# Kernel optimization log

Measured on AMD Instinct MI355X. Metric: run time of the kernel, lower is better.

Reference implementation:

```python
import jax, jax.numpy as jnp
import numpy as np

B, NPG, DEG = 16, 2048, 16          # graphs, nodes per graph, avg degree
N_TOT = B * NPG
E_TOT = N_TOT * DEG
NEG_SLOPE = 0.2


def _gat(x, src, dst, n, w, a_src, a_dst, b):
    # PyG GATConv: concat heads, add self loops, leaky_relu(0.2), segment softmax over targets
    H, C = a_src.shape
    h = (x @ w.T).reshape(n, H, C)                       # [n,H,C]
    sl = jnp.arange(n, dtype=src.dtype)
    s = jnp.concatenate([src, sl])
    d = jnp.concatenate([dst, sl])
    e = jax.nn.leaky_relu((h * a_src).sum(-1)[s] + (h * a_dst).sum(-1)[d], NEG_SLOPE)  # [E+n,H]
    emax = jax.lax.stop_gradient(jax.ops.segment_max(e, d, num_segments=n))
    ee = jnp.exp(e - emax[d])
    alpha = ee / (jax.ops.segment_sum(ee, d, num_segments=n)[d] + 1e-16)
    out = jax.ops.segment_sum(alpha[:, :, None] * h[s], d, num_segments=n)  # [n,H,C]
    return out.reshape(n, H * C) + b


def _gcn(x, src, dst, mask, n, w, b):
    # PyG GCNConv with self loops + symmetric norm; mask = float edge validity
    h = x @ w.T
    deg = jax.ops.segment_sum(mask, dst, num_segments=n) + 1.0  # +1 for self loop
    dinv = jax.lax.rsqrt(deg)
    coef = dinv[src] * dinv[dst] * mask
    out = jax.ops.segment_sum(coef[:, None] * h[src], dst, num_segments=n) + (dinv * dinv)[:, None] * h
    return out + b


def _sag(x, src, dst, mask, b_graphs, npg, k, w_rel, b_rel, w_root):
    # PyG SAGPooling(ratio=0.5): GraphConv score, per-graph top-k, x[perm]*tanh(score[perm]), filter_adj
    n = b_graphs * npg
    agg = jax.ops.segment_sum(mask[:, None] * x[src], dst, num_segments=n)
    score = (agg @ w_rel.T + b_rel + x @ w_root.T)[:, 0]      # [n]
    _, idx = jax.lax.top_k(score.reshape(b_graphs, npg), k)    # [B,k]
    perm = (jnp.arange(b_graphs, dtype=jnp.int32)[:, None] * npg + idx).reshape(-1)
    x_new = x[perm] * jnp.tanh(score[perm])[:, None]
    new_id = jnp.full((n,), -1, jnp.int32).at[perm].set(jnp.arange(b_graphs * k, dtype=jnp.int32))
    ns, nd = new_id[src], new_id[dst]
    valid = mask * ((ns >= 0) & (nd >= 0)).astype(x.dtype)
    return x_new, jnp.maximum(ns, 0), jnp.maximum(nd, 0), valid


def setup_inputs() -> dict:
    key = jax.random.key(0)
    ks = jax.random.split(key, 32)

    def lin(k, o, i):
        return (jax.random.normal(k, (o, i), jnp.float32) / np.sqrt(i)).astype(jnp.float32)

    x = jax.random.normal(ks[0], (N_TOT, 64), jnp.float32)
    off = jnp.repeat(jnp.arange(B, dtype=jnp.int32) * NPG, NPG * DEG)
    src = off + jax.random.randint(ks[1], (E_TOT,), 0, NPG, jnp.int32)
    dst = off + jax.random.randint(ks[2], (E_TOT,), 0, NPG, jnp.int32)
    edge_index = jnp.stack([src, dst])
    batch = jnp.repeat(jnp.arange(B, dtype=jnp.int32), NPG)

    return {
        'x': x, 'edge_index': edge_index, 'batch': batch,
        'gat1_w': lin(ks[3], 256, 64), 'gat1_asrc': lin(ks[4], 4, 64), 'gat1_adst': lin(ks[5], 4, 64),
        'gat1_b': jnp.zeros((256,), jnp.float32),
        'gat2_w': lin(ks[6], 256, 256), 'gat2_asrc': lin(ks[7], 4, 64), 'gat2_adst': lin(ks[8], 4, 64),
        'gat2_b': jnp.zeros((256,), jnp.float32),
        # pooling GCN1: 256 -> 128
        'gcn1_w': lin(ks[9], 128, 256), 'gcn1_b': jnp.zeros((128,), jnp.float32),
        'sag1_wrel': lin(ks[10], 1, 128), 'sag1_brel': jnp.zeros((1,), jnp.float32), 'sag1_wroot': lin(ks[11], 1, 128),
        # pooling GCN2: 128 -> 128
        'gcn2_w': lin(ks[12], 128, 128), 'gcn2_b': jnp.zeros((128,), jnp.float32),
        'sag2_wrel': lin(ks[13], 1, 128), 'sag2_brel': jnp.zeros((1,), jnp.float32), 'sag2_wroot': lin(ks[14], 1, 128),
        # classifier 128 -> 256 -> 128 -> 10
        'fc1_w': lin(ks[15], 256, 128), 'fc1_b': jnp.zeros((256,), jnp.float32),
        'fc2_w': lin(ks[16], 128, 256), 'fc2_b': jnp.zeros((128,), jnp.float32),
        'out_w': lin(ks[17], 10, 128), 'out_b': jnp.zeros((10,), jnp.float32),
    }


def reference(x, edge_index, batch,
              gat1_w, gat1_asrc, gat1_adst, gat1_b,
              gat2_w, gat2_asrc, gat2_adst, gat2_b,
              gcn1_w, gcn1_b, sag1_wrel, sag1_brel, sag1_wroot,
              gcn2_w, gcn2_b, sag2_wrel, sag2_brel, sag2_wroot,
              fc1_w, fc1_b, fc2_w, fc2_b, out_w, out_b):
    n = x.shape[0]
    src, dst = edge_index[0], edge_index[1]
    ones = jnp.ones(src.shape[0], x.dtype)

    # GAT encoder
    h = jax.nn.relu(_gat(x, src, dst, n, gat1_w, gat1_asrc, gat1_adst, gat1_b))
    h = _gat(h, src, dst, n, gat2_w, gat2_asrc, gat2_adst, gat2_b)  # [n,256]

    # GCN + SAGPool x2
    h = jax.nn.relu(_gcn(h, src, dst, ones, n, gcn1_w, gcn1_b))
    k1 = NPG // 2
    h, s1, d1, m1 = _sag(h, src, dst, ones, B, NPG, k1, sag1_wrel, sag1_brel, sag1_wroot)
    h = jax.nn.relu(_gcn(h, s1, d1, m1, B * k1, gcn2_w, gcn2_b))
    k2 = k1 // 2
    h, s2, d2, m2 = _sag(h, s1, d1, m1, B, k1, k2, sag2_wrel, sag2_brel, sag2_wroot)

    # global mean pool (equal-size graphs -> simple reshape-mean; batch vec implied)
    g = h.reshape(B, k2, -1).mean(axis=1)  # [B,128]

    # classifier MLP
    g = jax.nn.relu(g @ fc1_w.T + fc1_b)
    g = jax.nn.relu(g @ fc2_w.T + fc2_b)
    return g @ out_w.T + out_b  # [B,10]
```

## Files before the change

### kernel.cpp

```cpp
#include <hip/hip_runtime.h>

#define N1 32768
#define EE 524288
#define NB 16
#define DEG 16
#define NPG1 2048
#define KK1 1024
#define N2 16384
#define NPG2 1024
#define KK2 512
#define N3 8192

typedef _Float16 half8_t __attribute__((ext_vector_type(8)));
typedef float floatx16 __attribute__((ext_vector_type(16)));

static __device__ __forceinline__ float leaky(float x){ return fmaxf(x, 0.2f*x); }

__global__ void count_dst(const int* __restrict__ dst, int* __restrict__ cnt, int E){
    int i = blockIdx.x*blockDim.x + threadIdx.x;
    if (i < E) atomicAdd(&cnt[dst[i]], 1);
}

__global__ void remap_count(const int* __restrict__ src, const int* __restrict__ dst,
                            const int* __restrict__ nid, int* __restrict__ ns,
                            int* __restrict__ nd, int* __restrict__ cnt, int E){
    int i = blockIdx.x*blockDim.x + threadIdx.x;
    if (i < E){
        int a = nid[src[i]], b = nid[dst[i]];
        ns[i] = a; nd[i] = b;
        if (a >= 0 && b >= 0) atomicAdd(&cnt[b], 1);
    }
}

__global__ void blocksum_k(const int* __restrict__ cnt, int* __restrict__ bs){
    __shared__ int red[4];
    int tid = threadIdx.x;
    int v = cnt[blockIdx.x*256 + tid];
    #pragma unroll
    for (int off = 32; off; off >>= 1) v += __shfl_xor(v, off);
    if ((tid & 63) == 0) red[tid >> 6] = v;
    __syncthreads();
    if (tid == 0) bs[blockIdx.x] = red[0] + red[1] + red[2] + red[3];
}

__global__ void scan_write_k(const int* __restrict__ cnt, const int* __restrict__ bs,
                             int nb, int2* __restrict__ rpx, int* __restrict__ cur,
                             float* __restrict__ dinv){
    __shared__ int sbs[128];
    __shared__ int wsum[4];
    int tid = threadIdx.x;
    int b = blockIdx.x;
    if (tid < nb) sbs[tid] = bs[tid];
    __syncthreads();
    for (int off = 1; off < nb; off <<= 1){
        int v = 0;
        if (tid < nb && tid >= off) v = sbs[tid - off];
        __syncthreads();
        if (tid < nb) sbs[tid] += v;
        __syncthreads();
    }
    int base = (b == 0) ? 0 : sbs[b-1];
    int i = b*256 + tid;
    int c = cnt[i];
    int lane = tid & 63, wv = tid >> 6;
    int x = c;
    #pragma unroll
    for (int off = 1; off < 64; off <<= 1){ int y = __shfl_up(x, off); if (lane >= off) x += y; }
    if (lane == 63) wsum[wv] = x;
    __syncthreads();
    if (tid == 0){ int run = 0; for (int w2 = 0; w2 < 4; w2++){ int t = wsum[w2]; wsum[w2] = run; run += t; } }
    __syncthreads();
    int excl = x - c + wsum[wv];
    int beg = base + excl;
    rpx[i]  = make_int2(beg, beg + c);
    cur[i]  = beg;
    dinv[i] = rsqrtf((float)c + 1.0f);
}

__global__ void scatter1(const int* __restrict__ src, const int* __restrict__ dst,
                         int* __restrict__ cur, int* __restrict__ esrc, int E){
    int i = blockIdx.x*blockDim.x + threadIdx.x;
    if (i < E){ int p = atomicAdd(&cur[dst[i]], 1); esrc[p] = src[i]; }
}

__global__ void scatter2(const int* __restrict__ ns, const int* __restrict__ nd,
                         int* __restrict__ cur, int* __restrict__ esrc, int E){
    int i = blockIdx.x*blockDim.x + threadIdx.x;
    if (i < E){
        int a = ns[i], b = nd[i];
        if (a >= 0 && b >= 0){ int p = atomicAdd(&cur[b], 1); esrc[p] = a; }
    }
}

__global__ void wsplit4(const float* __restrict__ w0, int n0,
                        const float* __restrict__ w1, int n1,
                        const float* __restrict__ w2, int n2,
                        const float* __restrict__ w3, int n3,
                        _Float16* __restrict__ wh, _Float16* __restrict__ wl){
    int i = blockIdx.x*256 + threadIdx.x;
    int n01 = n0 + n1, n012 = n01 + n2, nt = n012 + n3;
    if (i >= nt) return;
    float v = (i < n0) ? w0[i] : (i < n01) ? w1[i - n0] : (i < n012) ? w2[i - n01] : w3[i - n012];
    _Float16 h = (_Float16)v;
    wh[i] = h; wl[i] = (_Float16)(v - (float)h);
}

#define KS 64
static __device__ __forceinline__ int ldsoff(int row, int k8){
    return row*64 + ((k8 ^ (row & 7)) << 3);
}

__global__ __launch_bounds__(256, 2) void gemm_h2(const float* __restrict__ A,
        const _Float16* __restrict__ WHp, const _Float16* __restrict__ WLp,
        float* __restrict__ C, int n, int K, int M,
        const int* __restrict__ perm, const float* __restrict__ tt){
    __shared__ _Float16 sm[4*128*KS];
    _Float16* sAH = sm;
    _Float16* sAL = sm + 128*KS;
    _Float16* sWH = sm + 2*128*KS;
    _Float16* sWL = sm + 3*128*KS;
    int t = threadIdx.x;
    int lane = t & 63;
    int wid = t >> 6;
    int wr = wid >> 1, wc = wid & 1;
    int row0 = blockIdx.x*128, col0 = blockIdx.y*128;
    int srow = t >> 3;
    int sk8  = t & 7;

    floatx16 acc[2][2];
    #pragma unroll
    for (int i = 0; i < 2; i++)
        #pragma unroll
        for (int j = 0; j < 2; j++)
            #pragma unroll
            for (int q = 0; q < 16; q++) acc[i][j][q] = 0.f;

    for (int kk = 0; kk < K; kk += KS){
        #pragma unroll
        for (int p = 0; p < 4; p++){
            int r = srow + p*32;
            int rr = row0 + r;
            int arow = perm ? perm[rr] : rr;
            float tscale = perm ? tt[rr] : 1.0f;
            const float* ga = A + (size_t)arow*K + kk + sk8*8;
            float4 a0 = *(const float4*)ga;
            float4 a1 = *(const float4*)(ga + 4);
            half8_t ahi, alo;
            float av[8] = {a0.x,a0.y,a0.z,a0.w,a1.x,a1.y,a1.z,a1.w};
            #pragma unroll
            for (int q = 0; q < 8; q++){
                float v = av[q] * tscale;
                _Float16 h = (_Float16)v;
                ahi[q] = h; alo[q] = (_Float16)(v - (float)h);
            }
            size_t wo = (size_t)(col0 + r)*K + kk + sk8*8;
            half8_t whi = *(const half8_t*)(WHp + wo);
            half8_t wlo = *(const half8_t*)(WLp + wo);
            int o = ldsoff(r, sk8);
            *(half8_t*)&sAH[o] = ahi;
            *(half8_t*)&sAL[o] = alo;
            *(half8_t*)&sWH[o] = whi;
            *(half8_t*)&sWL[o] = wlo;
        }
        __syncthreads();
        #pragma unroll
        for (int kc = 0; kc < 4; kc++){
            int k8 = kc*2 + (lane >> 5);
            int ra = wr*64 + (lane & 31);
            int rb = wc*64 + (lane & 31);
            half8_t ah0 = *(const half8_t*)&sAH[ldsoff(ra,      k8)];
            half8_t ah1 = *(const half8_t*)&sAH[ldsoff(ra + 32, k8)];
            half8_t al0 = *(const half8_t*)&sAL[ldsoff(ra,      k8)];
            half8_t al1 = *(const half8_t*)&sAL[ldsoff(ra + 32, k8)];
            half8_t bh0 = *(const half8_t*)&sWH[ldsoff(rb,      k8)];
            half8_t bh1 = *(const half8_t*)&sWH[ldsoff(rb + 32, k8)];
            half8_t bl0 = *(const half8_t*)&sWL[ldsoff(rb,      k8)];
            half8_t bl1 = *(const half8_t*)&sWL[ldsoff(rb + 32, k8)];
            acc[0][0] = __builtin_amdgcn_mfma_f32_32x32x16_f16(ah0, bh0, acc[0][0], 0,0,0);
            acc[0][0] = __builtin_amdgcn_mfma_f32_32x32x16_f16(ah0, bl0, acc[0][0], 0,0,0);
            acc[0][0] = __builtin_amdgcn_mfma_f32_32x32x16_f16(al0, bh0, acc[0][0], 0,0,0);
            acc[0][1] = __builtin_amdgcn_mfma_f32_32x32x16_f16(ah0, bh1, acc[0][1], 0,0,0);
            acc[0][1] = __builtin_amdgcn_mfma_f32_32x32x16_f16(ah0, bl1, acc[0][1], 0,0,0);
            acc[0][1] = __builtin_amdgcn_mfma_f32_32x32x16_f16(al0, bh1, acc[0][1], 0,0,0);
            acc[1][0] = __builtin_amdgcn_mfma_f32_32x32x16_f16(ah1, bh0, acc[1][0], 0,0,0);
            acc[1][0] = __builtin_amdgcn_mfma_f32_32x32x16_f16(ah1, bl0, acc[1][0], 0,0,0);
            acc[1][0] = __builtin_amdgcn_mfma_f32_32x32x16_f16(al1, bh0, acc[1][0], 0,0,0);
            acc[1][1] = __builtin_amdgcn_mfma_f32_32x32x16_f16(ah1, bh1, acc[1][1], 0,0,0);
            acc[1][1] = __builtin_amdgcn_mfma_f32_32x32x16_f16(ah1, bl1, acc[1][1], 0,0,0);
            acc[1][1] = __builtin_amdgcn_mfma_f32_32x32x16_f16(al1, bh1, acc[1][1], 0,0,0);
        }
        __syncthreads();
    }
    #pragma unroll
    for (int rt = 0; rt < 2; rt++)
        #pragma unroll
        for (int ct = 0; ct < 2; ct++){
            int baser = row0 + wr*64 + rt*32 + 4*(lane >> 5);
            int c = col0 + wc*64 + ct*32 + (lane & 31);
            #pragma unroll
            for (int r = 0; r < 16; r++){
                int rr = baser + (r & 3) + 8*(r >> 2);
                C[(size_t)rr*M + c] = acc[rt][ct][r];
            }
        }
}

__global__ void attn_pre(const float* __restrict__ h, const float* __restrict__ wsrc,
                         const float* __restrict__ wdst, float* __restrict__ as_,
                         float* __restrict__ ad_){
    int lane = threadIdx.x & 63;
    int w = threadIdx.x >> 6;
    int d = blockIdx.x*4 + w;
    float4 hv = *(const float4*)(h + (size_t)d*256 + lane*4);
    float4 ws = *(const float4*)(wsrc + lane*4);
    float4 wd = *(const float4*)(wdst + lane*4);
    float ps = hv.x*ws.x + hv.y*ws.y + hv.z*ws.z + hv.w*ws.w;
    float pd = hv.x*wd.x + hv.y*wd.y + hv.z*wd.z + hv.w*wd.w;
    #pragma unroll
    for (int m = 8; m; m >>= 1){ ps += __shfl_xor(ps, m); pd += __shfl_xor(pd, m); }
    if ((lane & 15) == 0){
        as_[d*4 + (lane >> 4)] = ps;
        ad_[d*4 + (lane >> 4)] = pd;
    }
}

template<int RELU>
__global__ void gat_agg(const float* __restrict__ h, const float* __restrict__ as_,
                        const float* __restrict__ ad_, const float* __restrict__ bias,
                        const int2* __restrict__ rpx, const int* __restrict__ esrc,
                        float* __restrict__ out){
    int lane = threadIdx.x & 63;
    int nb = gridDim.x;
    int b = blockIdx.x;
    int sb = (b & 7)*(nb >> 3) + (b >> 3);
    int d = __builtin_amdgcn_readfirstlane(sb*4 + (int)(threadIdx.x >> 6));
    int2 re = rpx[d];
    int beg = re.x, end = re.y;

    int hh = lane >> 4;
    float adh = ad_[(d<<2) + hh];
    float aself = as_[(d<<2) + hh];

    float dn[4];
    dn[0] = __expf(leaky(aself + adh)); dn[1] = 0.f; dn[2] = 0.f; dn[3] = 0.f;
    float4 hd = ((const float4*)(h + ((size_t)d<<8)))[lane];
    float4 AX[4];
    AX[0].x = dn[0]*hd.x; AX[0].y = dn[0]*hd.y; AX[0].z = dn[0]*hd.z; AX[0].w = dn[0]*hd.w;
    AX[1] = {0,0,0,0}; AX[2] = {0,0,0,0}; AX[3] = {0,0,0,0};

    int i = beg;
    int endu = beg + ((end - beg) & ~7);
    for (; i < endu; i += 8){
        int s_[8];
        #pragma unroll
        for (int j = 0; j < 8; j++) s_[j] = __builtin_amdgcn_readfirstlane(esrc[i + j]);
        float a_[8];
        #pragma unroll
        for (int j = 0; j < 8; j++) a_[j] = as_[(s_[j]<<2) + hh];
        float4 hv_[8];
        #pragma unroll
        for (int j = 0; j < 8; j++) hv_[j] = ((const float4*)(h + ((size_t)s_[j]<<8)))[lane];
        #pragma unroll
        for (int j = 0; j < 8; j++){
            float x = a_[j] + adh;
            float p = __expf(fmaxf(x, 0.2f*x));
            dn[j & 3] += p;
            AX[j & 3].x = fmaf(p, hv_[j].x, AX[j & 3].x);
            AX[j & 3].y = fmaf(p, hv_[j].y, AX[j & 3].y);
            AX[j & 3].z = fmaf(p, hv_[j].z, AX[j & 3].z);
            AX[j & 3].w = fmaf(p, hv_[j].w, AX[j & 3].w);
        }
    }
    for (; i < end; ++i){
        int s = __builtin_amdgcn_readfirstlane(esrc[i]);
        float x = as_[(s<<2) + hh] + adh;
        float4 hv = ((const float4*)(h + ((size_t)s<<8)))[lane];
        float p = __expf(fmaxf(x, 0.2f*x));
        dn[0] += p;
        AX[0].x = fmaf(p, hv.x, AX[0].x); AX[0].y = fmaf(p, hv.y, AX[0].y);
        AX[0].z = fmaf(p, hv.z, AX[0].z); AX[0].w = fmaf(p, hv.w, AX[0].w);
    }
    float den = ((dn[0] + dn[1]) + (dn[2] + dn[3])) + 1e-16f;
    float r = 1.0f / den;
    int c0 = lane*4;
    float4 bv = *(const float4*)(bias + c0);
    float4 acc;
    acc.x = ((AX[0].x+AX[1].x)+(AX[2].x+AX[3].x))*r + bv.x;
    acc.y = ((AX[0].y+AX[1].y)+(AX[2].y+AX[3].y))*r + bv.y;
    acc.z = ((AX[0].z+AX[1].z)+(AX[2].z+AX[3].z))*r + bv.z;
    acc.w = ((AX[0].w+AX[1].w)+(AX[2].w+AX[3].w))*r + bv.w;
    if (RELU){
        acc.x = fmaxf(acc.x, 0.f); acc.y = fmaxf(acc.y, 0.f);
        acc.z = fmaxf(acc.z, 0.f); acc.w = fmaxf(acc.w, 0.f);
    }
    ((float4*)(out + ((size_t)d<<8)))[lane] = acc;
}

__global__ void gcn_agg_sag(const float* __restrict__ h, const float* __restrict__ dinv,
                            const float* __restrict__ bias,
                            const float* __restrict__ wrel, const float* __restrict__ wroot,
                            const float* __restrict__ brel,
                            const int2* __restrict__ rpx, const int* __restrict__ esrc,
                            float* __restrict__ out, float* __restrict__ Y, float* __restrict__ Z){
    int lane = threadIdx.x & 63;
    int nb = gridDim.x;
    int b = blockIdx.x;
    int sb = (b & 7)*(nb >> 3) + (b >> 3);
    int d = __builtin_amdgcn_readfirstlane(sb*4 + (int)(threadIdx.x >> 6));
    int2 re = rpx[d];
    int beg = re.x, end = re.y;
    float dv = dinv[d];
    int c0 = lane*2;
    float2 hd = ((const float2*)(h + ((size_t)d<<7)))[lane];
    float self = dv*dv;
    float ax[4] = {self*hd.x, 0.f, 0.f, 0.f};
    float ay[4] = {self*hd.y, 0.f, 0.f, 0.f};
    int i = beg;
    int endu = beg + ((end - beg) & ~7);
    for (; i < endu; i += 8){
        int s_[8];
        #pragma unroll
        for (int j = 0; j < 8; j++) s_[j] = __builtin_amdgcn_readfirstlane(esrc[i + j]);
        float di_[8];
        #pragma unroll
        for (int j = 0; j < 8; j++) di_[j] = dinv[s_[j]];
        float2 hv_[8];
        #pragma unroll
        for (int j = 0; j < 8; j++) hv_[j] = ((const float2*)(h + ((size_t)s_[j]<<7)))[lane];
        #pragma unroll
        for (int j = 0; j < 8; j++){
            float coef = di_[j]*dv;
            ax[j & 3] = fmaf(coef, hv_[j].x, ax[j & 3]);
            ay[j & 3] = fmaf(coef, hv_[j].y, ay[j & 3]);
        }
    }
    for (; i < end; ++i){
        int s = __builtin_amdgcn_readfirstlane(esrc[i]);
        float coef = dinv[s]*dv;
        float2 hv = ((const float2*)(h + ((size_t)s<<7)))[lane];
        ax[0] = fmaf(coef, hv.x, ax[0]); ay[0] = fmaf(coef, hv.y, ay[0]);
    }
    float axs = ((ax[0]+ax[1])+(ax[2]+ax[3]));
    float ays = ((ay[0]+ay[1])+(ay[2]+ay[3]));
    axs = fmaxf(axs + bias[c0], 0.f);
    ays = fmaxf(ays + bias[c0+1], 0.f);
    float2 o; o.x = axs; o.y = ays;
    ((float2*)(out + ((size_t)d<<7)))[lane] = o;
    float py = axs*wrel[c0]  + ays*wrel[c0+1];
    float pz = axs*wroot[c0] + ays*wroot[c0+1];
    #pragma unroll
    for (int off = 32; off; off >>= 1){ py += __shfl_xor(py, off); pz += __shfl_xor(pz, off); }
    if (lane == 0){ Y[d] = py; Z[d] = pz + brel[0]; }
}

__global__ void sag_lite(const float* __restrict__ Y, const float* __restrict__ Z,
                         const int2* __restrict__ rpx, const int* __restrict__ esrc,
                         float* __restrict__ score){
    int lane = threadIdx.x & 63;
    int w = threadIdx.x >> 6;
    int nb = gridDim.x;
    int b = blockIdx.x;
    int sb = (b & 7)*(nb >> 3) + (b >> 3);
    int d = sb*4 + w;
    int2 re = rpx[d];
    float s = 0.f;
    for (int i = re.x + lane; i < re.y; i += 64) s += Y[esrc[i]];
    #pragma unroll
    for (int off = 32; off; off >>= 1) s += __shfl_xor(s, off);
    if (lane == 0) score[d] = s + Z[d];
}

__global__ __launch_bounds__(64) void topk_wave(const float* __restrict__ score,
        int npg, int k, int* __restrict__ perm, float* __restrict__ ssort,
        int* __restrict__ nid, int writeNid){
    __shared__ unsigned keys[2048];
    __shared__ int hist[256];
    int g = blockIdx.x;
    int lane = threadIdx.x;
    int nch = npg >> 6;
    for (int c = 0; c < nch; c++){
        unsigned u = __float_as_uint(score[g*npg + c*64 + lane]);
        keys[c*64 + lane] = (u & 0x80000000u) ? ~u : (u | 0x80000000u);
    }
    int need = k;
    unsigned prefix = 0u, pmask = 0u;
    #pragma unroll
    for (int shift = 24; shift >= 0; shift -= 8){
        #pragma unroll
        for (int q = 0; q < 4; q++) hist[lane*4 + q] = 0;
        for (int c = 0; c < nch; c++){
            unsigned u = keys[c*64 + lane];
            if ((u & pmask) == prefix) atomicAdd(&hist[(u >> shift) & 255u], 1);
        }
        int h0 = hist[lane*4], h1 = hist[lane*4+1], h2 = hist[lane*4+2], h3 = hist[lane*4+3];
        int s3 = h3, s2 = h2 + s3, s1 = h1 + s2, s0 = h0 + s1;
        int tot = s0;
        int suf = tot;
        #pragma unroll
        for (int off = 1; off < 64; off <<= 1){
            int v = __shfl_down(suf, off);
            if (lane + off < 64) suf += v;
        }
        int above_quad = suf - tot;
        int c0 = s0 + above_quad, c1 = s1 + above_quad, c2 = s2 + above_quad, c3 = s3 + above_quad;
        int sel = -1;
        if (c0 >= need && c1 < need) sel = 0;
        if (c1 >= need && c2 < need) sel = 1;
        if (c2 >= need && c3 < need) sel = 2;
        if (c3 >= need && above_quad < need) sel = 3;
        unsigned long long msk = __ballot(sel >= 0);
        int srcl = __ffsll((long long)msk) - 1;
        int binq = __shfl(sel, srcl);
        int bin = srcl*4 + binq;
        int cge_next = (binq == 0) ? __shfl(c1, srcl) :
                       (binq == 1) ? __shfl(c2, srcl) :
                       (binq == 2) ? __shfl(c3, srcl) : __shfl(above_quad, srcl);
        need -= cge_next;
        prefix |= ((unsigned)bin) << shift;
        pmask  |= 255u << shift;
    }
    unsigned thr = prefix;
    int m = need;
    unsigned long long below = (lane == 63) ? 0x7FFFFFFFFFFFFFFFull : ((1ull << lane) - 1ull);
    int base = 0, eqbase = 0;
    for (int c = 0; c < nch; c++){
        unsigned u = keys[c*64 + lane];
        bool gt = u > thr;
        bool eq = (u == thr);
        unsigned long long meq = __ballot(eq);
        int eqrank = eqbase + __popcll(meq & below);
        bool take = gt || (eq && eqrank < m);
        unsigned long long mtk = __ballot(take);
        int pos = base + __popcll(mtk & below);
        int node = g*npg + c*64 + lane;
        if (take){
            perm[g*k + pos] = node;
            ssort[g*k + pos] = tanhf(score[node]);
            if (writeNid) nid[node] = g*k + pos;
        } else if (writeNid) nid[node] = -1;
        base += __popcll(mtk);
        eqbase += __popcll(meq);
    }
}

__global__ void pool_mean2(const float* __restrict__ x, const int* __restrict__ perm,
                           const float* __restrict__ ssort, float* __restrict__ g){
    __shared__ float tt[KK2];
    __shared__ float part[128];
    int b = blockIdx.x, t = threadIdx.x;
    tt[t]       = ssort[b*KK2 + t];
    tt[t + 256] = ssort[b*KK2 + t + 256];
    __syncthreads();
    int c = t & 127, half = t >> 7;
    float s = 0.f;
    #pragma unroll 4
    for (int i = half*256; i < half*256 + 256; i++){
        int o = perm[b*KK2 + i];
        s = fmaf(tt[i], x[(size_t)o*128 + c], s);
    }
    if (half) part[c] = s;
    __syncthreads();
    if (!half) g[b*128 + c] = (s + part[c]) * (1.0f/KK2);
}

__global__ void mlp_k(const float* __restrict__ g,
                      const float* __restrict__ fc1w, const float* __restrict__ fc1b,
                      const float* __restrict__ fc2w, const float* __restrict__ fc2b,
                      const float* __restrict__ ow,  const float* __restrict__ ob,
                      float* __restrict__ out){
    __shared__ float gv[128], t1[256], t2[128];
    int b = blockIdx.x, t = threadIdx.x;
    if (t < 128) gv[t] = g[b*128 + t];
    __syncthreads();
    {
        float s = fc1b[t];
        for (int c = 0; c < 128; c++) s += gv[c]*fc1w[t*128 + c];
        t1[t] = fmaxf(s, 0.f);
    }
    __syncthreads();
    if (t < 128){
        float s = fc2b[t];
        for (int c = 0; c < 256; c++) s += t1[c]*fc2w[t*256 + c];
        t2[t] = fmaxf(s, 0.f);
    }
    __syncthreads();
    if (t < 10){
        float s = ob[t];
        for (int c = 0; c < 128; c++) s += t2[c]*ow[t*128 + c];
        out[b*10 + t] = s;
    }
}

extern "C" void kernel_launch(void* const* d_in, const int* in_sizes, int n_in,
                              void* d_out, int out_size, void* d_ws, size_t ws_size,
                              hipStream_t stream){
    (void)in_sizes; (void)n_in; (void)out_size; (void)ws_size;
    const float* x    = (const float*)d_in[0];
    const int*   eidx = (const int*)d_in[1];
    const int*   src  = eidx;
    const int*   dst  = eidx + EE;
    const float* g1w  = (const float*)d_in[3];
    const float* g1as = (const float*)d_in[4];
    const float* g1ad = (const float*)d_in[5];
    const float* g1b  = (const float*)d_in[6];
    const float* g2w  = (const float*)d_in[7];
    const float* g2as = (const float*)d_in[8];
    const float* g2ad = (const float*)d_in[9];
    const float* g2b  = (const float*)d_in[10];
    const float* c1w  = (const float*)d_in[11];
    const float* c1b  = (const float*)d_in[12];
    const float* s1wrel  = (const float*)d_in[13];
    const float* s1brel  = (const float*)d_in[14];
    const float* s1wroot = (const float*)d_in[15];
    const float* c2w  = (const float*)d_in[16];
    const float* c2b  = (const float*)d_in[17];
    const float* s2wrel  = (const float*)d_in[18];
    const float* s2brel  = (const float*)d_in[19];
    const float* s2wroot = (const float*)d_in[20];
    const float* f1w  = (const float*)d_in[21];
    const float* f1b  = (const float*)d_in[22];
    const float* f2w  = (const float*)d_in[23];
    const float* f2b  = (const float*)d_in[24];
    const float* ow   = (const float*)d_in[25];
    const float* ob   = (const float*)d_in[26];
    float* out = (float*)d_out;

    char* ws = (char*)d_ws;
    size_t off = 0;
    auto alloc = [&](size_t bytes)->char*{
        char* p = ws + off;
        off += (bytes + 255) & ~(size_t)255;
        return p;
    };
    float* F0     = (float*)alloc((size_t)N1*256*4);
    float* F1     = (float*)alloc((size_t)N1*256*4);
    float* F2     = (float*)alloc((size_t)N2*128*4);
    float* AS     = (float*)alloc((size_t)N1*4*4);
    float* AD     = (float*)alloc((size_t)N1*4*4);
    int2*  RPX    = (int2*) alloc((size_t)N1*8);
    int*   CUR    = (int*)  alloc((size_t)N1*4);
    int*   EL     = (int*)  alloc((size_t)EE*4);
    float* DINV   = (float*)alloc((size_t)N1*4);
    float* SCORE  = (float*)alloc((size_t)N1*4);
    float* Y      = (float*)alloc((size_t)N1*4);
    float* Z      = (float*)alloc((size_t)N1*4);
    int*   PERM1  = (int*)  alloc((size_t)N2*4);
    float* SSORT1 = (float*)alloc((size_t)N2*4);
    int*   NID    = (int*)  alloc((size_t)N1*4);
    int*   E1S    = (int*)  alloc((size_t)EE*4);
    int*   E1D    = (int*)  alloc((size_t)EE*4);
    int2*  RPX2   = (int2*) alloc((size_t)N2*8);
    int*   CUR2   = (int*)  alloc((size_t)N2*4);
    int*   EL2    = (int*)  alloc((size_t)EE*4);
    float* DINV2  = (float*)alloc((size_t)N2*4);
    int*   PERM2  = (int*)  alloc((size_t)N3*4);
    float* SSORT2 = (float*)alloc((size_t)N3*4);
    float* GBUF   = (float*)alloc((size_t)NB*128*4);
    int*   BS     = (int*)  alloc((size_t)128*4);
    _Float16* WH  = (_Float16*)alloc((size_t)131072*2);
    _Float16* WL  = (_Float16*)alloc((size_t)131072*2);
    const int o_g1 = 0, o_g2 = 16384, o_c1 = 81920, o_c2 = 114688;

    hipMemsetAsync(CUR, 0, (size_t)N1*4, stream);
    count_dst<<<EE/256, 256, 0, stream>>>(dst, CUR, EE);
    blocksum_k<<<N1/256, 256, 0, stream>>>(CUR, BS);
    scan_write_k<<<N1/256, 256, 0, stream>>>(CUR, BS, N1/256, RPX, CUR, DINV);
    scatter1<<<EE/256, 256, 0, stream>>>(src, dst, CUR, EL, EE);
    wsplit4<<<512, 256, 0, stream>>>(g1w, 16384, g2w, 65536, c1w, 32768, c2w, 16384, WH, WL);

    gemm_h2<<<dim3(N1/128, 2), 256, 0, stream>>>(x, WH + o_g1, WL + o_g1, F0, N1, 64, 256, nullptr, nullptr);
    attn_pre<<<N1/4, 256, 0, stream>>>(F0, g1as, g1ad, AS, AD);
    gat_agg<1><<<N1/4, 256, 0, stream>>>(F0, AS, AD, g1b, RPX, EL, F1);

    gemm_h2<<<dim3(N1/128, 2), 256, 0, stream>>>(F1, WH + o_g2, WL + o_g2, F0, N1, 256, 256, nullptr, nullptr);
    attn_pre<<<N1/4, 256, 0, stream>>>(F0, g2as, g2ad, AS, AD);
    gat_agg<0><<<N1/4, 256, 0, stream>>>(F0, AS, AD, g2b, RPX, EL, F1);

    gemm_h2<<<dim3(N1/128, 1), 256, 0, stream>>>(F1, WH + o_c1, WL + o_c1, F0, N1, 256, 128, nullptr, nullptr);
    gcn_agg_sag<<<N1/4, 256, 0, stream>>>(F0, DINV, c1b, s1wrel, s1wroot, s1brel,
                                          RPX, EL, F1, Y, Z);

    sag_lite<<<N1/4, 256, 0, stream>>>(Y, Z, RPX, EL, SCORE);
    topk_wave<<<NB, 64, 0, stream>>>(SCORE, NPG1, KK1, PERM1, SSORT1, NID, 1);

    hipMemsetAsync(CUR2, 0, (size_t)N2*4, stream);
    remap_count<<<EE/256, 256, 0, stream>>>(src, dst, NID, E1S, E1D, CUR2, EE);
    blocksum_k<<<N2/256, 256, 0, stream>>>(CUR2, BS);
    scan_write_k<<<N2/256, 256, 0, stream>>>(CUR2, BS, N2/256, RPX2, CUR2, DINV2);
    scatter2<<<EE/256, 256, 0, stream>>>(E1S, E1D, CUR2, EL2, EE);

    gemm_h2<<<dim3(N2/128, 1), 256, 0, stream>>>(F1, WH + o_c2, WL + o_c2, F0, N2, 128, 128, PERM1, SSORT1);
    gcn_agg_sag<<<N2/4, 256, 0, stream>>>(F0, DINV2, c2b, s2wrel, s2wroot, s2brel,
                                          RPX2, EL2, F2, Y, Z);

    sag_lite<<<N2/4, 256, 0, stream>>>(Y, Z, RPX2, EL2, SCORE);
    topk_wave<<<NB, 64, 0, stream>>>(SCORE, NPG2, KK2, PERM2, SSORT2, nullptr, 0);

    pool_mean2<<<NB, 256, 0, stream>>>(F2, PERM2, SSORT2, GBUF);
    mlp_k<<<NB, 256, 0, stream>>>(GBUF, f1w, f1b, f2w, f2b, ow, ob, out);
}
```

Before: 335.5 us.

## Build pooled CSR directly from first CSR and fuse small launches

The second-level CSR is now built by filtering each kept node's existing neighbor list through the node-id map, one wave per destination node. This replaces the remap/count/scan/scatter sequence, which took several full-edge passes plus atomics. The count kernel also absorbs the weight-split work as extra blocks, and pooling is merged with the MLP, removing launches and a memset. The new CSR keeps the old row offsets, so rows are sparse with gaps, and edge order within a row follows the original CSR rather than atomic order.

Result: faster. 314.8 us (-6.2%).

```diff
diff --git a/kernel.cpp b/kernel.cpp
--- a/kernel.cpp
+++ b/kernel.cpp
@@ -16,19 +16,23 @@
 
 static __device__ __forceinline__ float leaky(float x){ return fmaxf(x, 0.2f*x); }
 
-__global__ void count_dst(const int* __restrict__ dst, int* __restrict__ cnt, int E){
-    int i = blockIdx.x*blockDim.x + threadIdx.x;
-    if (i < E) atomicAdd(&cnt[dst[i]], 1);
-}
-
-__global__ void remap_count(const int* __restrict__ src, const int* __restrict__ dst,
-                            const int* __restrict__ nid, int* __restrict__ ns,
-                            int* __restrict__ nd, int* __restrict__ cnt, int E){
-    int i = blockIdx.x*blockDim.x + threadIdx.x;
-    if (i < E){
-        int a = nid[src[i]], b = nid[dst[i]];
-        ns[i] = a; nd[i] = b;
-        if (a >= 0 && b >= 0) atomicAdd(&cnt[b], 1);
+__global__ void count_split(const int* __restrict__ dst, int* __restrict__ cnt,
+                            const float* __restrict__ w0, int n0,
+                            const float* __restrict__ w1, int n1,
+                            const float* __restrict__ w2, int n2,
+                            const float* __restrict__ w3, int n3,
+                            _Float16* __restrict__ wh, _Float16* __restrict__ wl){
+    int b = blockIdx.x;
+    int tid = threadIdx.x;
+    if (b < EE/256){
+        atomicAdd(&cnt[dst[b*256 + tid]], 1);
+    } else {
+        int i = (b - EE/256)*256 + tid;
+        int n01 = n0 + n1, n012 = n01 + n2, nt = n012 + n3;
+        if (i >= nt) return;
+        float v = (i < n0) ? w0[i] : (i < n01) ? w1[i - n0] : (i < n012) ? w2[i - n01] : w3[i - n012];
+        _Float16 h = (_Float16)v;
+        wh[i] = h; wl[i] = (_Float16)(v - (float)h);
     }
 }
 
@@ -83,26 +87,32 @@
     if (i < E){ int p = atomicAdd(&cur[dst[i]], 1); esrc[p] = src[i]; }
 }
 
-__global__ void scatter2(const int* __restrict__ ns, const int* __restrict__ nd,
-                         int* __restrict__ cur, int* __restrict__ esrc, int E){
-    int i = blockIdx.x*blockDim.x + threadIdx.x;
-    if (i < E){
-        int a = ns[i], b = nd[i];
-        if (a >= 0 && b >= 0){ int p = atomicAdd(&cur[b], 1); esrc[p] = a; }
-    }
-}
-
-__global__ void wsplit4(const float* __restrict__ w0, int n0,
-                        const float* __restrict__ w1, int n1,
-                        const float* __restrict__ w2, int n2,
-                        const float* __restrict__ w3, int n3,
-                        _Float16* __restrict__ wh, _Float16* __restrict__ wl){
-    int i = blockIdx.x*256 + threadIdx.x;
-    int n01 = n0 + n1, n012 = n01 + n2, nt = n012 + n3;
-    if (i >= nt) return;
-    float v = (i < n0) ? w0[i] : (i < n01) ? w1[i - n0] : (i < n012) ? w2[i - n01] : w3[i - n012];
-    _Float16 h = (_Float16)v;
-    wh[i] = h; wl[i] = (_Float16)(v - (float)h);
+__global__ void csr2_build(const int* __restrict__ perm, const int* __restrict__ nid,
+                           const int2* __restrict__ rpx, const int* __restrict__ EL,
+                           int2* __restrict__ rpx2, float* __restrict__ dinv2,
+                           int* __restrict__ EL2){
+    int lane = threadIdx.x & 63;
+    int w = threadIdx.x >> 6;
+    int d2 = blockIdx.x*4 + w;
+    int old = __builtin_amdgcn_readfirstlane(perm[d2]);
+    int2 re = rpx[old];
+    int beg = re.x, end = re.y;
+    unsigned long long below = (1ull << lane) - 1ull;
+    int cnt = 0;
+    for (int i = beg; i < end; i += 64){
+        int ii = i + lane;
+        int sn = -1;
+        if (ii < end) sn = nid[EL[ii]];
+        bool take = sn >= 0;
+        unsigned long long m = __ballot(take);
+        int pos = cnt + __popcll(m & below);
+        if (take) EL2[beg + pos] = sn;
+        cnt += __popcll(m);
+    }
+    if (lane == 0){
+        rpx2[d2] = make_int2(beg, beg + cnt);
+        dinv2[d2] = rsqrtf((float)cnt + 1.0f);
+    }
 }
 
 #define KS 64
@@ -443,10 +453,15 @@
     }
 }
 
-__global__ void pool_mean2(const float* __restrict__ x, const int* __restrict__ perm,
-                           const float* __restrict__ ssort, float* __restrict__ g){
+__global__ void pool_mlp(const float* __restrict__ x, const int* __restrict__ perm,
+                         const float* __restrict__ ssort,
+                         const float* __restrict__ fc1w, const float* __restrict__ fc1b,
+                         const float* __restrict__ fc2w, const float* __restrict__ fc2b,
+                         const float* __restrict__ ow,  const float* __restrict__ ob,
+                         float* __restrict__ out){
     __shared__ float tt[KK2];
     __shared__ float part[128];
+    __shared__ float gv[128], t1[256], t2[128];
     int b = blockIdx.x, t = threadIdx.x;
     tt[t]       = ssort[b*KK2 + t];
     tt[t + 256] = ssort[b*KK2 + t + 256];
@@ -460,34 +475,24 @@
     }
     if (half) part[c] = s;
     __syncthreads();
-    if (!half) g[b*128 + c] = (s + part[c]) * (1.0f/KK2);
-}
-
-__global__ void mlp_k(const float* __restrict__ g,
-                      const float* __restrict__ fc1w, const float* __restrict__ fc1b,
-                      const float* __restrict__ fc2w, const float* __restrict__ fc2b,
-                      const float* __restrict__ ow,  const float* __restrict__ ob,
-                      float* __restrict__ out){
-    __shared__ float gv[128], t1[256], t2[128];
-    int b = blockIdx.x, t = threadIdx.x;
-    if (t < 128) gv[t] = g[b*128 + t];
+    if (!half) gv[c] = (s + part[c]) * (1.0f/KK2);
     __syncthreads();
     {
-        float s = fc1b[t];
-        for (int c = 0; c < 128; c++) s += gv[c]*fc1w[t*128 + c];
-        t1[t] = fmaxf(s, 0.f);
+        float s1 = fc1b[t];
+        for (int cc = 0; cc < 128; cc++) s1 += gv[cc]*fc1w[t*128 + cc];
+        t1[t] = fmaxf(s1, 0.f);
     }
     __syncthreads();
     if (t < 128){
-        float s = fc2b[t];
-        for (int c = 0; c < 256; c++) s += t1[c]*fc2w[t*256 + c];
-        t2[t] = fmaxf(s, 0.f);
+        float s2 = fc2b[t];
+        for (int cc = 0; cc < 256; cc++) s2 += t1[cc]*fc2w[t*256 + cc];
+        t2[t] = fmaxf(s2, 0.f);
     }
     __syncthreads();
     if (t < 10){
-        float s = ob[t];
-        for (int c = 0; c < 128; c++) s += t2[c]*ow[t*128 + c];
-        out[b*10 + t] = s;
+        float s3 = ob[t];
+        for (int cc = 0; cc < 128; cc++) s3 += t2[cc]*ow[t*128 + cc];
+        out[b*10 + t] = s3;
     }
 }
 
@@ -547,26 +552,22 @@
     int*   PERM1  = (int*)  alloc((size_t)N2*4);
     float* SSORT1 = (float*)alloc((size_t)N2*4);
     int*   NID    = (int*)  alloc((size_t)N1*4);
-    int*   E1S    = (int*)  alloc((size_t)EE*4);
-    int*   E1D    = (int*)  alloc((size_t)EE*4);
     int2*  RPX2   = (int2*) alloc((size_t)N2*8);
-    int*   CUR2   = (int*)  alloc((size_t)N2*4);
     int*   EL2    = (int*)  alloc((size_t)EE*4);
     float* DINV2  = (float*)alloc((size_t)N2*4);
     int*   PERM2  = (int*)  alloc((size_t)N3*4);
     float* SSORT2 = (float*)alloc((size_t)N3*4);
-    float* GBUF   = (float*)alloc((size_t)NB*128*4);
     int*   BS     = (int*)  alloc((size_t)128*4);
     _Float16* WH  = (_Float16*)alloc((size_t)131072*2);
     _Float16* WL  = (_Float16*)alloc((size_t)131072*2);
     const int o_g1 = 0, o_g2 = 16384, o_c1 = 81920, o_c2 = 114688;
 
     hipMemsetAsync(CUR, 0, (size_t)N1*4, stream);
-    count_dst<<<EE/256, 256, 0, stream>>>(dst, CUR, EE);
+    count_split<<<EE/256 + 512, 256, 0, stream>>>(dst, CUR,
+        g1w, 16384, g2w, 65536, c1w, 32768, c2w, 16384, WH, WL);
     blocksum_k<<<N1/256, 256, 0, stream>>>(CUR, BS);
     scan_write_k<<<N1/256, 256, 0, stream>>>(CUR, BS, N1/256, RPX, CUR, DINV);
     scatter1<<<EE/256, 256, 0, stream>>>(src, dst, CUR, EL, EE);
-    wsplit4<<<512, 256, 0, stream>>>(g1w, 16384, g2w, 65536, c1w, 32768, c2w, 16384, WH, WL);
 
     gemm_h2<<<dim3(N1/128, 2), 256, 0, stream>>>(x, WH + o_g1, WL + o_g1, F0, N1, 64, 256, nullptr, nullptr);
     attn_pre<<<N1/4, 256, 0, stream>>>(F0, g1as, g1ad, AS, AD);
@@ -583,11 +584,7 @@
     sag_lite<<<N1/4, 256, 0, stream>>>(Y, Z, RPX, EL, SCORE);
     topk_wave<<<NB, 64, 0, stream>>>(SCORE, NPG1, KK1, PERM1, SSORT1, NID, 1);
 
-    hipMemsetAsync(CUR2, 0, (size_t)N2*4, stream);
-    remap_count<<<EE/256, 256, 0, stream>>>(src, dst, NID, E1S, E1D, CUR2, EE);
-    blocksum_k<<<N2/256, 256, 0, stream>>>(CUR2, BS);
-    scan_write_k<<<N2/256, 256, 0, stream>>>(CUR2, BS, N2/256, RPX2, CUR2, DINV2);
-    scatter2<<<EE/256, 256, 0, stream>>>(E1S, E1D, CUR2, EL2, EE);
+    csr2_build<<<N2/4, 256, 0, stream>>>(PERM1, NID, RPX, EL, RPX2, DINV2, EL2);
 
     gemm_h2<<<dim3(N2/128, 1), 256, 0, stream>>>(F1, WH + o_c2, WL + o_c2, F0, N2, 128, 128, PERM1, SSORT1);
     gcn_agg_sag<<<N2/4, 256, 0, stream>>>(F0, DINV2, c2b, s2wrel, s2wroot, s2brel,
@@ -596,6 +593,6 @@
     sag_lite<<<N2/4, 256, 0, stream>>>(Y, Z, RPX2, EL2, SCORE);
     topk_wave<<<NB, 64, 0, stream>>>(SCORE, NPG2, KK2, PERM2, SSORT2, nullptr, 0);
 
-    pool_mean2<<<NB, 256, 0, stream>>>(F2, PERM2, SSORT2, GBUF);
-    mlp_k<<<NB, 256, 0, stream>>>(GBUF, f1w, f1b, f2w, f2b, ow, ob, out);
-}
+    pool_mlp<<<NB, 256, 0, stream>>>(F2, PERM2, SSORT2,
+                                     f1w, f1b, f2w, f2b, ow, ob, out);
+}
```
